# Kernel tuning notes

Hardware: AMD Instinct MI355X
Metric: run time of the kernel (lower is better)

Reference implementation:

```python
import jax, jax.numpy as jnp
import numpy as np

# dims
N, T, DIN = 256, 32, 2048      # batch, time, gpt output dim
H = 2048                        # MLP hidden
G, C, D = 2, 16, 256            # vq groups, codebook size, code dim
W, A = 5, 7                     # action window, action dim
WA = W * A                      # output_size
DEC_H = 512                     # vqvae decoder hidden
NT = N * T


def _mk(key, shape, scale=0.02):
    return jax.random.normal(key, shape, dtype=jnp.float32) * scale


def setup_inputs() -> dict:
    key = jax.random.key(0)
    ks = jax.random.split(key, 16)
    inp = {
        "x": jax.random.normal(ks[0], (N, T, DIN), dtype=jnp.float32),
        # bin1 MLP: DIN -> H -> H -> C
        "w11": _mk(ks[1], (DIN, H)), "b11": jnp.zeros((H,), jnp.float32),
        "w12": _mk(ks[2], (H, H)),   "b12": jnp.zeros((H,), jnp.float32),
        "w13": _mk(ks[3], (H, C)),   "b13": jnp.zeros((C,), jnp.float32),
        # bin2 MLP: DIN+C -> H -> C
        "w21": _mk(ks[4], (DIN + C, H)), "b21": jnp.zeros((H,), jnp.float32),
        "w22": _mk(ks[5], (H, C)),       "b22": jnp.zeros((C,), jnp.float32),
        # offset MLP: DIN -> H -> H -> G*C*WA
        "wo1": _mk(ks[6], (DIN, H)), "bo1": jnp.zeros((H,), jnp.float32),
        "wo2": _mk(ks[7], (H, H)),   "bo2": jnp.zeros((H,), jnp.float32),
        "wo3": _mk(ks[8], (H, G * C * WA)), "bo3": jnp.zeros((G * C * WA,), jnp.float32),
        # residual-VQ codebooks: (G, C, D)
        "codebook": _mk(ks[9], (G, C, D), scale=1.0),
        # frozen vqvae decoder: G*D -> DEC_H -> WA
        "wd1": _mk(ks[10], (G * D, DEC_H)), "bd1": jnp.zeros((DEC_H,), jnp.float32),
        "wd2": _mk(ks[11], (DEC_H, WA)),    "bd2": jnp.zeros((WA,), jnp.float32),
    }
    return inp


def reference(x, w11, b11, w12, b12, w13, b13, w21, b21, w22, b22,
              wo1, bo1, wo2, bo2, wo3, bo3, codebook, wd1, bd1, wd2, bd2):
    xf = x.reshape(NT, DIN)
    # bin1 logits
    h = jax.nn.relu(xf @ w11 + b11)
    h = jax.nn.relu(h @ w12 + b12)
    cbet_logits1 = h @ w13 + b13                       # (NT, C)
    # offsets
    o = jax.nn.relu(xf @ wo1 + bo1)
    o = jax.nn.relu(o @ wo2 + bo2)
    cbet_offsets = (o @ wo3 + bo3).reshape(NT, G, C, WA)
    # multinomial sampling (== categorical over softmax(logits))
    key = jax.random.key(42)
    k1, k2 = jax.random.split(key)
    s1 = jax.random.categorical(k1, cbet_logits1)      # (NT,)
    one_hot1 = jax.nn.one_hot(s1, C, dtype=xf.dtype)
    h2 = jax.nn.relu(jnp.concatenate([xf, one_hot1], axis=1) @ w21 + b21)
    cbet_logits2 = h2 @ w22 + b22                      # (NT, C)
    s2 = jax.random.categorical(k2, cbet_logits2)
    sampled_centers = jnp.stack([s1, s2], axis=1)      # (NT, G)
    # gather offsets at sampled codes, sum over groups
    nt_idx = jnp.arange(NT)[:, None]
    g_idx = jnp.arange(G)[None, :]
    sampled_offsets = cbet_offsets[nt_idx, g_idx, sampled_centers].sum(axis=1)  # (NT, WA)
    # vq codebook lookup + frozen decoder (detached in torch)
    centers = codebook[g_idx, sampled_centers]          # (NT, G, D)
    dec_in = jax.lax.stop_gradient(centers.reshape(NT, G * D))
    decoded = jax.nn.relu(dec_in @ wd1 + bd1) @ wd2 + bd2
    decoded = jax.lax.stop_gradient(decoded)            # (NT, WA)
    predicted = (decoded.reshape(NT, W, A) + sampled_offsets.reshape(NT, W, A))
    predicted_action = predicted.reshape(N, T, WA)
    return predicted_action, decoded, cbet_logits1, cbet_logits2, sampled_centers
```

## Files before the change

kernel.cpp:

```cpp
#include <hip/hip_runtime.h>
#include <cstdint>
#include <cstddef>

#define NT_   8192
#define DIN_  2048
#define H_    2048
#define C_    16
#define G_    2
#define D_    256
#define WA_   35
#define DECH_ 512
#define NPAD_ 1152

typedef _Float16 f16;
typedef _Float16 h4 __attribute__((ext_vector_type(4)));
typedef _Float16 h8 __attribute__((ext_vector_type(8)));
typedef float fx4 __attribute__((ext_vector_type(4)));

typedef __attribute__((address_space(1))) const void gvoid_t;
typedef __attribute__((address_space(3))) void lvoid_t;

__device__ __forceinline__ void gld16(const void* g, void* l) {
  __builtin_amdgcn_global_load_lds((gvoid_t*)(uintptr_t)g,
                                   (lvoid_t*)(uint32_t)(uintptr_t)l, 16, 0, 0);
}

template <int N>
__device__ __forceinline__ void waitvm() {
  if constexpr (N == 8)      asm volatile("s_waitcnt vmcnt(8)" ::: "memory");
  else if constexpr (N == 6) asm volatile("s_waitcnt vmcnt(6)" ::: "memory");
  else if constexpr (N == 4) asm volatile("s_waitcnt vmcnt(4)" ::: "memory");
  else if constexpr (N == 2) asm volatile("s_waitcnt vmcnt(2)" ::: "memory");
  else                       asm volatile("s_waitcnt vmcnt(0)" ::: "memory");
}

__host__ __device__ inline void tf2x32(uint32_t k0, uint32_t k1,
                                       uint32_t x0, uint32_t x1,
                                       uint32_t& o0, uint32_t& o1) {
  const uint32_t ks2 = k0 ^ k1 ^ 0x1BD11BDAu;
  uint32_t ks[3] = {k0, k1, ks2};
  x0 += ks[0]; x1 += ks[1];
  const uint32_t R0[4] = {13u, 15u, 26u, 6u};
  const uint32_t R1[4] = {17u, 29u, 16u, 24u};
#pragma unroll
  for (int g = 0; g < 5; ++g) {
    const uint32_t* R = (g & 1) ? R1 : R0;
#pragma unroll
    for (int r = 0; r < 4; ++r) {
      x0 += x1;
      x1 = (x1 << R[r]) | (x1 >> (32u - R[r]));
      x1 ^= x0;
    }
    x0 += ks[(g + 1) % 3];
    x1 += ks[(g + 2) % 3] + (uint32_t)(g + 1);
  }
  o0 = x0; o1 = x1;
}

template <int TERMS, int RELU, int GATHER, int WLO, int ACONV>
__global__ __launch_bounds__(512, 2) void gemm256(
    const void* __restrict__ Ahi_, const void* __restrict__ Alo_,
    const f16* __restrict__ Bhi, const f16* __restrict__ Blo,
    const float* __restrict__ bias,
    f16* __restrict__ Chi, f16* __restrict__ Clo,
    int M, int N, int K,
    const int* __restrict__ gidx, const float* __restrict__ growp, int gldw) {
  extern __shared__ f16 lds[];
  constexpr int NREG = (TERMS == 3) ? 4 : 2;
  constexpr int BS   = NREG * 8192;
  constexpr int NGLD = (TERMS == 3) ? (ACONV ? 4 : 8) : (ACONV ? 2 : 4);

  const int tid  = threadIdx.x;
  const int wave = tid >> 6;
  const int lane = tid & 63;
  const int lr   = lane & 15;

  const int nb  = N >> 8;
  const int nwg = (int)gridDim.x;
  const int qq  = nwg >> 3;
  const int sw  = ((int)blockIdx.x & 7) * qq + ((int)blockIdx.x >> 3);
  const int by  = sw / nb, bx = sw % nb;
  const int m0  = by << 8, n0 = bx << 8;

  const int wm = (wave >> 2) * 128;
  const int wn = (wave & 3) * 64;

  fx4 acc[8][4];
#pragma unroll
  for (int i = 0; i < 8; ++i)
#pragma unroll
    for (int j = 0; j < 4; ++j) acc[i][j] = (fx4){0.f, 0.f, 0.f, 0.f};

  const int r_row = wave * 16 + (lane >> 2);
  const int r_g   = (lane & 3) ^ ((lane >> 3) & 3);
  const f16* gsrc[NGLD];
  int gdst[NGLD];
  {
    int nr = 0;
    auto AR = [&](const f16* P, int mn, int reg, int rb) {
      gsrc[nr] = P + (size_t)(mn + rb + r_row) * K + r_g * 8;
      gdst[nr] = reg * 8192 + rb * 32 + wave * 512;
      ++nr;
    };
    if constexpr (TERMS == 3) {
      if constexpr (!ACONV) {
        AR((const f16*)Ahi_, m0, 0, 0); AR((const f16*)Ahi_, m0, 0, 128);
        AR((const f16*)Alo_, m0, 1, 0); AR((const f16*)Alo_, m0, 1, 128);
      }
      AR(Bhi, n0, 2, 0); AR(Bhi, n0, 2, 128);
      AR(Blo, n0, 3, 0); AR(Blo, n0, 3, 128);
    } else {
      if constexpr (!ACONV) {
        AR((const f16*)Ahi_, m0, 0, 0); AR((const f16*)Ahi_, m0, 0, 128);
      }
      AR(Bhi, n0, 1, 0); AR(Bhi, n0, 1, 128);
    }
  }

  const float* A32 = (const float*)Ahi_;
  const float* psrc[4];
  int pdst[4];
  if constexpr (ACONV) {
#pragma unroll
    for (int p = 0; p < 4; ++p) {
      const int e4 = tid + p * 512;
      const int arow = e4 >> 3;
      psrc[p] = A32 + (size_t)(m0 + arow) * K + (e4 & 7) * 4;
      const int phys = ((e4 >> 1) & 3) ^ ((e4 >> 4) & 3);
      pdst[p] = arow * 32 + phys * 8 + (e4 & 1) * 4;
    }
  }

  float4 pf[4];
  if constexpr (ACONV) {
#pragma unroll
    for (int p = 0; p < 4; ++p) pf[p] = *(const float4*)psrc[p];
  }
#pragma unroll
  for (int r = 0; r < NGLD; ++r) gld16(gsrc[r], lds + gdst[r]);

  const int KT  = K >> 5;
  const int pg8 = ((lane >> 4) ^ ((lr >> 1) & 3)) * 8;

  for (int t = 0; t < KT; ++t) {
    f16* const sb  = lds + (t & 1) * BS;
    f16* const nsb = lds + ((t + 1) & 1) * BS;
    const int ktn = (t + 1 < KT ? t + 1 : t) * 32;

    if constexpr (ACONV) {
#pragma unroll
      for (int p = 0; p < 4; ++p) {
        const float4 v = pf[p];
        h4 hh; hh.x = (f16)v.x; hh.y = (f16)v.y; hh.z = (f16)v.z; hh.w = (f16)v.w;
        *(h4*)(sb + pdst[p]) = hh;
        if constexpr (TERMS == 3) {
          h4 ll;
          ll.x = (f16)(v.x - (float)hh.x); ll.y = (f16)(v.y - (float)hh.y);
          ll.z = (f16)(v.z - (float)hh.z); ll.w = (f16)(v.w - (float)hh.w);
          *(h4*)(sb + 8192 + pdst[p]) = ll;
        }
      }
      asm volatile("s_waitcnt lgkmcnt(0)" ::: "memory");
    }
    if constexpr (ACONV) {
#pragma unroll
      for (int p = 0; p < 4; ++p) pf[p] = *(const float4*)(psrc[p] + ktn);
    }
#pragma unroll
    for (int r = 0; r < NGLD; ++r) gld16(gsrc[r] + ktn, nsb + gdst[r]);
    if constexpr (!ACONV) waitvm<NGLD>();
    __builtin_amdgcn_s_barrier();
    asm volatile("" ::: "memory");

    const f16* sAh = sb;
    const f16* sAl = sb + 8192;
    const f16* sBh = sb + (TERMS == 3 ? 2 : 1) * 8192;
    const f16* sBl = sb + 3 * 8192;

    h8 vbh[4], vbl[4];
#pragma unroll
    for (int j = 0; j < 4; ++j) {
      const int row = wn + j * 16 + lr;
      vbh[j] = *(const h8*)(sBh + row * 32 + pg8);
      if constexpr (TERMS == 3) vbl[j] = *(const h8*)(sBl + row * 32 + pg8);
    }
#pragma unroll
    for (int mq = 0; mq < 2; ++mq) {
      h8 va[4];
#pragma unroll
      for (int i = 0; i < 4; ++i)
        va[i] = *(const h8*)(sAh + (wm + mq * 64 + i * 16 + lr) * 32 + pg8);
      __builtin_amdgcn_s_setprio(1);
#pragma unroll
      for (int i = 0; i < 4; ++i)
#pragma unroll
        for (int j = 0; j < 4; ++j) {
          acc[mq * 4 + i][j] = __builtin_amdgcn_mfma_f32_16x16x32_f16(
              va[i], vbh[j], acc[mq * 4 + i][j], 0, 0, 0);
          if constexpr (TERMS == 3)
            acc[mq * 4 + i][j] = __builtin_amdgcn_mfma_f32_16x16x32_f16(
                va[i], vbl[j], acc[mq * 4 + i][j], 0, 0, 0);
        }
      __builtin_amdgcn_s_setprio(0);
      if constexpr (TERMS == 3) {
        h8 vl[4];
#pragma unroll
        for (int i = 0; i < 4; ++i)
          vl[i] = *(const h8*)(sAl + (wm + mq * 64 + i * 16 + lr) * 32 + pg8);
        __builtin_amdgcn_s_setprio(1);
#pragma unroll
        for (int i = 0; i < 4; ++i)
#pragma unroll
          for (int j = 0; j < 4; ++j)
            acc[mq * 4 + i][j] = __builtin_amdgcn_mfma_f32_16x16x32_f16(
                vl[i], vbh[j], acc[mq * 4 + i][j], 0, 0, 0);
        __builtin_amdgcn_s_setprio(0);
      }
    }
    __builtin_amdgcn_s_barrier();
    asm volatile("" ::: "memory");
  }

  const int rq = (lane >> 4) * 4;
#pragma unroll
  for (int mi = 0; mi < 8; ++mi) {
#pragma unroll
    for (int q = 0; q < 4; ++q) {
      const int row = m0 + wm + mi * 16 + rq + q;
      const float* gr = nullptr;
      if constexpr (GATHER) gr = growp + (size_t)gidx[row] * gldw;
#pragma unroll
      for (int j = 0; j < 4; ++j) {
        const int col = n0 + wn + j * 16 + lr;
        float v = acc[mi][j][q];
        if (bias) v += bias[col];
        if constexpr (GATHER) v += gr[col];
        if constexpr (RELU) v = fmaxf(v, 0.f);
        const f16 hh = (f16)v;
        Chi[(size_t)row * N + col] = hh;
        if constexpr (WLO) Clo[(size_t)row * N + col] = (f16)(v - (float)hh);
      }
    }
  }
}

template <int TERMS, int RELU, int GATHER, int WLO, int ACONV>
__global__ __launch_bounds__(256, 2) void gemm128(
    const void* __restrict__ Ahi_, const void* __restrict__ Alo_,
    const f16* __restrict__ Bhi, const f16* __restrict__ Blo,
    const float* __restrict__ bias,
    f16* __restrict__ Chi, f16* __restrict__ Clo,
    int M, int N, int K,
    const int* __restrict__ gidx, const float* __restrict__ growp, int gldw) {
  constexpr int NTILE = (TERMS == 3) ? 4 : 2;
  __shared__ f16 lds[NTILE * 4096];
  f16* sAh = lds;
  f16* sBh = lds + 4096;

  const int tid  = threadIdx.x;
  const int wave = tid >> 6;
  const int lane = tid & 63;
  const int n0 = blockIdx.x * 128;
  const int m0 = blockIdx.y * 128;
  const int wm = (wave >> 1) * 64;
  const int wn = (wave & 1) * 64;
  const int lr = lane & 15;
  const int lk = (lane >> 4) * 8;

  fx4 acc[4][4];
#pragma unroll
  for (int i = 0; i < 4; ++i)
#pragma unroll
    for (int j = 0; j < 4; ++j) acc[i][j] = (fx4){0.f, 0.f, 0.f, 0.f};

  const int sb = wave * 2048 + (lane << 4);

  for (int kt = 0; kt < K; kt += 32) {
#pragma unroll
    for (int c = 0; c < 2; ++c) {
      const int boff = sb + c * 1024;
      const int row  = boff >> 6;
      const int col  = (boff & 63) >> 1;
      gld16(Bhi + (size_t)(n0 + row) * K + kt + col, sBh + (wave * 2 + c) * 512);
      gld16(((const f16*)Ahi_) + (size_t)(m0 + row) * K + kt + col,
            sAh + (wave * 2 + c) * 512);
    }
    __syncthreads();

    h8 ah[4], bh[4];
#pragma unroll
    for (int t = 0; t < 4; ++t) {
      ah[t] = *(const h8*)&sAh[(wm + t * 16 + lr) * 32 + lk];
      bh[t] = *(const h8*)&sBh[(wn + t * 16 + lr) * 32 + lk];
    }
#pragma unroll
    for (int i = 0; i < 4; ++i)
#pragma unroll
      for (int j = 0; j < 4; ++j)
        acc[i][j] = __builtin_amdgcn_mfma_f32_16x16x32_f16(ah[i], bh[j], acc[i][j], 0, 0, 0);
    __syncthreads();
  }

  const int rq = (lane >> 4) * 4;
#pragma unroll
  for (int i = 0; i < 4; ++i) {
#pragma unroll
    for (int q = 0; q < 4; ++q) {
      const int row = m0 + wm + i * 16 + rq + q;
#pragma unroll
      for (int j = 0; j < 4; ++j) {
        const int col = n0 + wn + j * 16 + lr;
        float v = acc[i][j][q];
        if (bias) v += bias[col];
        if constexpr (RELU) v = fmaxf(v, 0.f);
        Chi[(size_t)row * N + col] = (f16)v;
      }
    }
  }
}

template <int SPLIT>
__global__ __launch_bounds__(256) void wtransT(
    const float* __restrict__ src, f16* __restrict__ hi, f16* __restrict__ lo,
    int K, int N, int Npad) {
  __shared__ float t[32][33];
  const int bn = blockIdx.x * 32;
  const int bk = blockIdx.y * 32;
  const int tx = threadIdx.x & 31, ty = threadIdx.x >> 5;
#pragma unroll
  for (int r = ty; r < 32; r += 8) {
    const float v = (bn + tx < N) ? src[(size_t)(bk + r) * N + bn + tx] : 0.f;
    t[tx][r] = v;
  }
  __syncthreads();
#pragma unroll
  for (int r = ty; r < 32; r += 8) {
    const float v = t[r][tx];
    const f16 hh = (f16)v;
    hi[(size_t)(bn + r) * K + bk + tx] = hh;
    if (SPLIT) lo[(size_t)(bn + r) * K + bk + tx] = (f16)(v - (float)hh);
  }
}

__global__ __launch_bounds__(256) void skinny16_hl(
    const f16* __restrict__ Ahi, const f16* __restrict__ Alo,
    const float* __restrict__ W, const float* __restrict__ bias,
    float* __restrict__ out) {
  __shared__ float row[H_];
  __shared__ float red[256];
  const int m = blockIdx.x;
  const f16* ah = Ahi + (size_t)m * H_;
  const f16* al = Alo + (size_t)m * H_;
  for (int i = threadIdx.x; i < H_ / 4; i += 256) {
    const h4 hh = ((const h4*)ah)[i];
    const h4 ll = ((const h4*)al)[i];
    row[i * 4 + 0] = (float)hh.x + (float)ll.x;
    row[i * 4 + 1] = (float)hh.y + (float)ll.y;
    row[i * 4 + 2] = (float)hh.z + (float)ll.z;
    row[i * 4 + 3] = (float)hh.w + (float)ll.w;
  }
  __syncthreads();
  const int c = threadIdx.x & 15, seg = threadIdx.x >> 4;
  const int k0 = seg * (H_ / 16);
  float p = 0.f;
  for (int i = 0; i < H_ / 16; ++i)
    p = fmaf(row[k0 + i], W[(size_t)(k0 + i) * C_ + c], p);
  red[threadIdx.x] = p;
  __syncthreads();
  if (threadIdx.x < C_) {
    float s = bias[threadIdx.x];
    for (int sg = 0; sg < 16; ++sg) s += red[sg * 16 + threadIdx.x];
    out[(size_t)m * C_ + threadIdx.x] = s;
  }
}

__global__ void sample_kernel(const float* __restrict__ logits,
                              int* __restrict__ s_out,
                              float* __restrict__ centers_out,
                              uint32_t ka, uint32_t kb, int which) {
  const int m = blockIdx.x * blockDim.x + threadIdx.x;
  if (m >= NT_) return;
  float best = -3.4e38f;
  int bi = 0;
#pragma unroll
  for (int c = 0; c < C_; ++c) {
    const uint32_t j = (uint32_t)(m * C_ + c);
    uint32_t o0, o1;
    tf2x32(ka, kb, 0u, j, o0, o1);
    const uint32_t bits = o0 ^ o1;
    const uint32_t fb = (bits >> 9) | 0x3f800000u;
    float u = __uint_as_float(fb) - 1.0f;
    u = fmaxf(1.17549435e-38f, u);
    const float gmb = -logf(-logf(u));
    const float z = gmb + logits[(size_t)m * C_ + c];
    if (z > best) { best = z; bi = c; }
  }
  s_out[m] = bi;
  centers_out[(size_t)m * G_ + which] = (float)bi;
}

__global__ void gather_dec_kernel(const float* __restrict__ codebook,
                                  const int* __restrict__ s1,
                                  const int* __restrict__ s2,
                                  f16* __restrict__ dec_in) {
  const int idx = blockIdx.x * blockDim.x + threadIdx.x;
  const int m = idx >> 9, d = idx & 511;
  const int g = d >> 8, dd = d & 255;
  const int s = g ? s2[m] : s1[m];
  dec_in[idx] = (f16)codebook[(size_t)(g * C_ + s) * D_ + dd];
}

__global__ __launch_bounds__(320) void final2(
    const f16* __restrict__ P,
    const float* __restrict__ bo3,
    const f16* __restrict__ dech,
    const float* __restrict__ wd2, const float* __restrict__ bd2,
    const int* __restrict__ s1, const int* __restrict__ s2,
    float* __restrict__ out_pred, float* __restrict__ out_dec) {
  __shared__ float drow[DECH_];
  const int m = blockIdx.x;
  for (int i = threadIdx.x; i < DECH_; i += 320)
    drow[i] = (float)dech[(size_t)m * DECH_ + i];
  __syncthreads();
  const int a1 = s1[m], a2 = s2[m];
  const int c = threadIdx.x >> 3, g = threadIdx.x & 7;
  float pdec = 0.f;
  if (c < WA_) {
    for (int i = 0; i < DECH_ / 8; ++i) {
      const int k = g * (DECH_ / 8) + i;
      pdec = fmaf(drow[k], wd2[(size_t)k * WA_ + c], pdec);
    }
  }
#pragma unroll
  for (int off = 1; off < 8; off <<= 1) pdec += __shfl_xor(pdec, off);
  if (c < WA_ && g == 0) {
    const float dec = pdec + bd2[c];
    const float soff = (float)P[(size_t)m * NPAD_ + a1 * WA_ + c]
                     + (float)P[(size_t)m * NPAD_ + C_ * WA_ + a2 * WA_ + c]
                     + bo3[a1 * WA_ + c] + bo3[C_ * WA_ + a2 * WA_ + c];
    out_dec[(size_t)m * WA_ + c] = dec;
    out_pred[(size_t)m * WA_ + c] = dec + soff;
  }
}

extern "C" void kernel_launch(void* const* d_in, const int* in_sizes, int n_in,
                              void* d_out, int out_size, void* d_ws, size_t ws_size,
                              hipStream_t stream) {
  const float* x    = (const float*)d_in[0];
  const float* w11  = (const float*)d_in[1];
  const float* b11  = (const float*)d_in[2];
  const float* w12  = (const float*)d_in[3];
  const float* b12  = (const float*)d_in[4];
  const float* w13  = (const float*)d_in[5];
  const float* b13  = (const float*)d_in[6];
  const float* w21  = (const float*)d_in[7];
  const float* b21  = (const float*)d_in[8];
  const float* w22  = (const float*)d_in[9];
  const float* b22  = (const float*)d_in[10];
  const float* wo1  = (const float*)d_in[11];
  const float* bo1  = (const float*)d_in[12];
  const float* wo2  = (const float*)d_in[13];
  const float* bo2  = (const float*)d_in[14];
  const float* wo3  = (const float*)d_in[15];
  const float* bo3  = (const float*)d_in[16];
  const float* cbk  = (const float*)d_in[17];
  const float* wd1  = (const float*)d_in[18];
  const float* bd1  = (const float*)d_in[19];
  const float* wd2  = (const float*)d_in[20];
  const float* bd2  = (const float*)d_in[21];

  float* out = (float*)d_out;
  float* out_pred = out;
  float* out_dec  = out + (size_t)NT_ * WA_;
  float* out_l1   = out + (size_t)2 * NT_ * WA_;
  float* out_l2   = out_l1 + (size_t)NT_ * C_;
  float* out_sc   = out_l2 + (size_t)NT_ * C_;

  const size_t AB = (size_t)NT_ * H_;
  f16* R0a = (f16*)d_ws;
  f16* R0b = R0a + AB;
  f16* R1a = R0b + AB;
  f16* R1b = R1a + AB;
  f16* WH  = R1b + AB;
  f16* WL  = WH + (size_t)H_ * H_;
  int* S1  = (int*)(WL + (size_t)H_ * H_);
  int* S2  = S1 + NT_;

  f16* P     = R1a;
  f16* DECIN = R0a;
  f16* DECH  = R0a + (size_t)NT_ * DECH_;

  hipFuncSetAttribute(reinterpret_cast<const void*>(&gemm256<3,1,0,1,1>),
                      hipFuncAttributeMaxDynamicSharedMemorySize, 131072);
  hipFuncSetAttribute(reinterpret_cast<const void*>(&gemm256<3,1,0,1,0>),
                      hipFuncAttributeMaxDynamicSharedMemorySize, 131072);
  hipFuncSetAttribute(reinterpret_cast<const void*>(&gemm256<3,1,1,1,1>),
                      hipFuncAttributeMaxDynamicSharedMemorySize, 131072);
  hipFuncSetAttribute(reinterpret_cast<const void*>(&gemm256<1,1,0,0,1>),
                      hipFuncAttributeMaxDynamicSharedMemorySize, 65536);
  hipFuncSetAttribute(reinterpret_cast<const void*>(&gemm256<1,1,0,0,0>),
                      hipFuncAttributeMaxDynamicSharedMemorySize, 65536);

  uint32_t k1a, k1b, k2a, k2b;
  tf2x32(0u, 42u, 0u, 0u, k1a, k1b);
  tf2x32(0u, 42u, 0u, 1u, k2a, k2b);

  const dim3 b256(256), b512(512);
  const dim3 gW(H_ / 32, H_ / 32);
  const dim3 gWo3(NPAD_ / 32, H_ / 32);
  const dim3 gWd1(DECH_ / 32, DECH_ / 32);
  const dim3 gBig((NT_ / 256) * (H_ / 256));
  const dim3 gP(NPAD_ / 128, NT_ / 128);
  const dim3 gD(DECH_ / 128, NT_ / 128);

  wtransT<1><<<gW, b256, 0, stream>>>(w11, WH, WL, H_, H_, H_);
  gemm256<3,1,0,1,1><<<gBig, b512, 131072, stream>>>(
      x, nullptr, WH, WL, b11, R0a, R0b, NT_, H_, DIN_, nullptr, nullptr, 0);
  wtransT<1><<<gW, b256, 0, stream>>>(w12, WH, WL, H_, H_, H_);
  gemm256<3,1,0,1,0><<<gBig, b512, 131072, stream>>>(
      R0a, R0b, WH, WL, b12, R1a, R1b, NT_, H_, H_, nullptr, nullptr, 0);
  skinny16_hl<<<NT_, 256, 0, stream>>>(R1a, R1b, w13, b13, out_l1);
  sample_kernel<<<NT_ / 256, 256, 0, stream>>>(out_l1, S1, out_sc, k1a, k1b, 0);

  wtransT<1><<<gW, b256, 0, stream>>>(w21, WH, WL, H_, H_, H_);
  gemm256<3,1,1,1,1><<<gBig, b512, 131072, stream>>>(
      x, nullptr, WH, WL, b21, R1a, R1b, NT_, H_, DIN_,
      S1, w21 + (size_t)DIN_ * H_, H_);
  skinny16_hl<<<NT_, 256, 0, stream>>>(R1a, R1b, w22, b22, out_l2);
  sample_kernel<<<NT_ / 256, 256, 0, stream>>>(out_l2, S2, out_sc, k2a, k2b, 1);

  wtransT<0><<<gW, b256, 0, stream>>>(wo1, WH, nullptr, H_, H_, H_);
  gemm256<1,1,0,0,1><<<gBig, b512, 65536, stream>>>(
      x, nullptr, WH, nullptr, bo1, R0a, nullptr, NT_, H_, DIN_, nullptr, nullptr, 0);
  wtransT<0><<<gW, b256, 0, stream>>>(wo2, WH, nullptr, H_, H_, H_);
  gemm256<1,1,0,0,0><<<gBig, b512, 65536, stream>>>(
      R0a, nullptr, WH, nullptr, bo2, R0b, nullptr, NT_, H_, H_, nullptr, nullptr, 0);
  wtransT<0><<<gWo3, b256, 0, stream>>>(wo3, WH, nullptr, H_, G_ * C_ * WA_, NPAD_);
  gemm128<1,0,0,0,0><<<gP, b256, 0, stream>>>(
      R0b, nullptr, WH, nullptr, nullptr, P, nullptr, NT_, NPAD_, H_, nullptr, nullptr, 0);

  gather_dec_kernel<<<(NT_ * DECH_) / 256, 256, 0, stream>>>(cbk, S1, S2, DECIN);
  wtransT<0><<<gWd1, b256, 0, stream>>>(wd1, WH, nullptr, DECH_, DECH_, DECH_);
  gemm128<1,1,0,0,0><<<gD, b256, 0, stream>>>(
      DECIN, nullptr, WH, nullptr, bd1, DECH, nullptr, NT_, DECH_, DECH_, nullptr, nullptr, 0);

  final2<<<NT_, 320, 0, stream>>>(P, bo3, DECH, wd2, bd2, S1, S2, out_pred, out_dec);

  (void)in_sizes; (void)n_in; (void)out_size; (void)ws_size;
}
```

Baseline: 1.102 ms.

## Pre-split x to fp16 pairs, fuse logit projection into GEMM epilogue, re-pipeline K loop

```diff
diff --git a/kernel.cpp b/kernel.cpp
--- a/kernel.cpp
+++ b/kernel.cpp
@@ -25,14 +25,13 @@
                                    (lvoid_t*)(uint32_t)(uintptr_t)l, 16, 0, 0);
 }
 
-template <int N>
-__device__ __forceinline__ void waitvm() {
-  if constexpr (N == 8)      asm volatile("s_waitcnt vmcnt(8)" ::: "memory");
-  else if constexpr (N == 6) asm volatile("s_waitcnt vmcnt(6)" ::: "memory");
-  else if constexpr (N == 4) asm volatile("s_waitcnt vmcnt(4)" ::: "memory");
-  else if constexpr (N == 2) asm volatile("s_waitcnt vmcnt(2)" ::: "memory");
-  else                       asm volatile("s_waitcnt vmcnt(0)" ::: "memory");
-}
+__device__ __forceinline__ void barrier_() {
+  asm volatile("" ::: "memory");
+  __builtin_amdgcn_s_barrier();
+  asm volatile("" ::: "memory");
+}
+
+#define MFMA_(d, a, b) d = __builtin_amdgcn_mfma_f32_16x16x32_f16(a, b, d, 0, 0, 0)
 
 __host__ __device__ inline void tf2x32(uint32_t k0, uint32_t k1,
                                        uint32_t x0, uint32_t x1,
@@ -57,18 +56,37 @@
   o0 = x0; o1 = x1;
 }
 
-template <int TERMS, int RELU, int GATHER, int WLO, int ACONV>
+__global__ __launch_bounds__(256) void xsplit_kernel(
+    const float* __restrict__ x, f16* __restrict__ xh, f16* __restrict__ xl) {
+  const size_t i = (size_t)blockIdx.x * 256 + threadIdx.x;
+  const float4 v0 = *(const float4*)(x + i * 8);
+  const float4 v1 = *(const float4*)(x + i * 8 + 4);
+  float vv[8] = {v0.x, v0.y, v0.z, v0.w, v1.x, v1.y, v1.z, v1.w};
+  h8 hh, ll;
+#pragma unroll
+  for (int k = 0; k < 8; ++k) {
+    const f16 h = (f16)vv[k];
+    hh[k] = h;
+    ll[k] = (f16)(vv[k] - (float)h);
+  }
+  *(h8*)(xh + i * 8) = hh;
+  *(h8*)(xl + i * 8) = ll;
+}
+
+enum { EPI_PAIR = 0, EPI_HI = 1, EPI_LOGIT = 2 };
+
+template <int TERMS, int GATHER, int EPI>
 __global__ __launch_bounds__(512, 2) void gemm256(
-    const void* __restrict__ Ahi_, const void* __restrict__ Alo_,
-    const f16* __restrict__ Bhi, const f16* __restrict__ Blo,
+    const f16* __restrict__ Ah, const f16* __restrict__ Al,
+    const f16* __restrict__ Bh, const f16* __restrict__ Bl,
     const float* __restrict__ bias,
     f16* __restrict__ Chi, f16* __restrict__ Clo,
     int M, int N, int K,
-    const int* __restrict__ gidx, const float* __restrict__ growp, int gldw) {
+    const int* __restrict__ gidx, const float* __restrict__ growp, int gldw,
+    const float* __restrict__ wlog, float* __restrict__ part) {
   extern __shared__ f16 lds[];
-  constexpr int NREG = (TERMS == 3) ? 4 : 2;
-  constexpr int BS   = NREG * 8192;
-  constexpr int NGLD = (TERMS == 3) ? (ACONV ? 4 : 8) : (ACONV ? 2 : 4);
+  constexpr int BS = ((TERMS == 3) ? 4 : 2) * 8192;
+  constexpr int NGLD = (TERMS == 3) ? 8 : 4;
 
   const int tid  = threadIdx.x;
   const int wave = tid >> 6;
@@ -103,157 +121,192 @@
       ++nr;
     };
     if constexpr (TERMS == 3) {
-      if constexpr (!ACONV) {
-        AR((const f16*)Ahi_, m0, 0, 0); AR((const f16*)Ahi_, m0, 0, 128);
-        AR((const f16*)Alo_, m0, 1, 0); AR((const f16*)Alo_, m0, 1, 128);
-      }
-      AR(Bhi, n0, 2, 0); AR(Bhi, n0, 2, 128);
-      AR(Blo, n0, 3, 0); AR(Blo, n0, 3, 128);
+      AR(Ah, m0, 0, 0); AR(Ah, m0, 0, 128);
+      AR(Al, m0, 1, 0); AR(Al, m0, 1, 128);
+      AR(Bh, n0, 2, 0); AR(Bh, n0, 2, 128);
+      AR(Bl, n0, 3, 0); AR(Bl, n0, 3, 128);
     } else {
-      if constexpr (!ACONV) {
-        AR((const f16*)Ahi_, m0, 0, 0); AR((const f16*)Ahi_, m0, 0, 128);
-      }
-      AR(Bhi, n0, 1, 0); AR(Bhi, n0, 1, 128);
-    }
-  }
-
-  const float* A32 = (const float*)Ahi_;
-  const float* psrc[4];
-  int pdst[4];
-  if constexpr (ACONV) {
-#pragma unroll
-    for (int p = 0; p < 4; ++p) {
-      const int e4 = tid + p * 512;
-      const int arow = e4 >> 3;
-      psrc[p] = A32 + (size_t)(m0 + arow) * K + (e4 & 7) * 4;
-      const int phys = ((e4 >> 1) & 3) ^ ((e4 >> 4) & 3);
-      pdst[p] = arow * 32 + phys * 8 + (e4 & 1) * 4;
-    }
-  }
-
-  float4 pf[4];
-  if constexpr (ACONV) {
-#pragma unroll
-    for (int p = 0; p < 4; ++p) pf[p] = *(const float4*)psrc[p];
-  }
+      AR(Ah, m0, 0, 0); AR(Ah, m0, 0, 128);
+      AR(Bh, n0, 1, 0); AR(Bh, n0, 1, 128);
+    }
+  }
+
 #pragma unroll
   for (int r = 0; r < NGLD; ++r) gld16(gsrc[r], lds + gdst[r]);
-
+  asm volatile("s_waitcnt vmcnt(0)" ::: "memory");
+  barrier_();
+
+  const int pg8 = ((lane >> 4) ^ ((lr >> 1) & 3)) * 8;
   const int KT  = K >> 5;
-  const int pg8 = ((lane >> 4) ^ ((lr >> 1) & 3)) * 8;
 
   for (int t = 0; t < KT; ++t) {
     f16* const sb  = lds + (t & 1) * BS;
     f16* const nsb = lds + ((t + 1) & 1) * BS;
     const int ktn = (t + 1 < KT ? t + 1 : t) * 32;
 
-    if constexpr (ACONV) {
-#pragma unroll
-      for (int p = 0; p < 4; ++p) {
-        const float4 v = pf[p];
-        h4 hh; hh.x = (f16)v.x; hh.y = (f16)v.y; hh.z = (f16)v.z; hh.w = (f16)v.w;
-        *(h4*)(sb + pdst[p]) = hh;
-        if constexpr (TERMS == 3) {
-          h4 ll;
-          ll.x = (f16)(v.x - (float)hh.x); ll.y = (f16)(v.y - (float)hh.y);
-          ll.z = (f16)(v.z - (float)hh.z); ll.w = (f16)(v.w - (float)hh.w);
-          *(h4*)(sb + 8192 + pdst[p]) = ll;
-        }
-      }
-      asm volatile("s_waitcnt lgkmcnt(0)" ::: "memory");
-    }
-    if constexpr (ACONV) {
-#pragma unroll
-      for (int p = 0; p < 4; ++p) pf[p] = *(const float4*)(psrc[p] + ktn);
-    }
-#pragma unroll
-    for (int r = 0; r < NGLD; ++r) gld16(gsrc[r] + ktn, nsb + gdst[r]);
-    if constexpr (!ACONV) waitvm<NGLD>();
-    __builtin_amdgcn_s_barrier();
-    asm volatile("" ::: "memory");
-
     const f16* sAh = sb;
     const f16* sAl = sb + 8192;
     const f16* sBh = sb + (TERMS == 3 ? 2 : 1) * 8192;
     const f16* sBl = sb + 3 * 8192;
 
-    h8 vbh[4], vbl[4];
+    h8 vbh[4], vbl[4], va[4];
 #pragma unroll
     for (int j = 0; j < 4; ++j) {
-      const int row = wn + j * 16 + lr;
-      vbh[j] = *(const h8*)(sBh + row * 32 + pg8);
-      if constexpr (TERMS == 3) vbl[j] = *(const h8*)(sBl + row * 32 + pg8);
-    }
-#pragma unroll
-    for (int mq = 0; mq < 2; ++mq) {
-      h8 va[4];
+      vbh[j] = *(const h8*)(sBh + (wn + j * 16 + lr) * 32 + pg8);
+      if constexpr (TERMS == 3)
+        vbl[j] = *(const h8*)(sBl + (wn + j * 16 + lr) * 32 + pg8);
+    }
+#pragma unroll
+    for (int i = 0; i < 4; ++i)
+      va[i] = *(const h8*)(sAh + (wm + i * 16 + lr) * 32 + pg8);
+    gld16(gsrc[0] + ktn, nsb + gdst[0]);
+    gld16(gsrc[1] + ktn, nsb + gdst[1]);
+    if constexpr (TERMS == 3) gld16(gsrc[2] + ktn, nsb + gdst[2]);
+    barrier_();
+    asm volatile("s_waitcnt lgkmcnt(0)" ::: "memory");
+    __builtin_amdgcn_sched_barrier(0);
+    __builtin_amdgcn_s_setprio(1);
+#pragma unroll
+    for (int i = 0; i < 4; ++i)
+#pragma unroll
+      for (int j = 0; j < 4; ++j) MFMA_(acc[i][j], va[i], vbh[j]);
+    if constexpr (TERMS == 3) {
 #pragma unroll
       for (int i = 0; i < 4; ++i)
-        va[i] = *(const h8*)(sAh + (wm + mq * 64 + i * 16 + lr) * 32 + pg8);
+#pragma unroll
+        for (int j = 0; j < 4; ++j) MFMA_(acc[i][j], va[i], vbl[j]);
+    }
+    __builtin_amdgcn_s_setprio(0);
+    barrier_();
+#pragma unroll
+    for (int i = 0; i < 4; ++i)
+      va[i] = *(const h8*)(sAh + (wm + 64 + i * 16 + lr) * 32 + pg8);
+    if constexpr (TERMS == 3) {
+      gld16(gsrc[3] + ktn, nsb + gdst[3]);
+      gld16(gsrc[4] + ktn, nsb + gdst[4]);
+      gld16(gsrc[5] + ktn, nsb + gdst[5]);
+    } else {
+      gld16(gsrc[2] + ktn, nsb + gdst[2]);
+      gld16(gsrc[3] + ktn, nsb + gdst[3]);
+    }
+    barrier_();
+    asm volatile("s_waitcnt lgkmcnt(0)" ::: "memory");
+    __builtin_amdgcn_sched_barrier(0);
+    __builtin_amdgcn_s_setprio(1);
+#pragma unroll
+    for (int i = 0; i < 4; ++i)
+#pragma unroll
+      for (int j = 0; j < 4; ++j) MFMA_(acc[4 + i][j], va[i], vbh[j]);
+    if constexpr (TERMS == 3) {
+#pragma unroll
+      for (int i = 0; i < 4; ++i)
+#pragma unroll
+        for (int j = 0; j < 4; ++j) MFMA_(acc[4 + i][j], va[i], vbl[j]);
+    }
+    __builtin_amdgcn_s_setprio(0);
+    if constexpr (TERMS != 3) asm volatile("s_waitcnt vmcnt(0)" ::: "memory");
+    barrier_();
+    if constexpr (TERMS == 3) {
+      h8 vl0[4], vl1[4];
+#pragma unroll
+      for (int i = 0; i < 4; ++i) {
+        vl0[i] = *(const h8*)(sAl + (wm + i * 16 + lr) * 32 + pg8);
+        vl1[i] = *(const h8*)(sAl + (wm + 64 + i * 16 + lr) * 32 + pg8);
+      }
+      gld16(gsrc[6] + ktn, nsb + gdst[6]);
+      gld16(gsrc[7] + ktn, nsb + gdst[7]);
+      barrier_();
+      asm volatile("s_waitcnt lgkmcnt(0)" ::: "memory");
+      __builtin_amdgcn_sched_barrier(0);
       __builtin_amdgcn_s_setprio(1);
 #pragma unroll
       for (int i = 0; i < 4; ++i)
 #pragma unroll
         for (int j = 0; j < 4; ++j) {
-          acc[mq * 4 + i][j] = __builtin_amdgcn_mfma_f32_16x16x32_f16(
-              va[i], vbh[j], acc[mq * 4 + i][j], 0, 0, 0);
-          if constexpr (TERMS == 3)
-            acc[mq * 4 + i][j] = __builtin_amdgcn_mfma_f32_16x16x32_f16(
-                va[i], vbl[j], acc[mq * 4 + i][j], 0, 0, 0);
+          MFMA_(acc[i][j], vl0[i], vbh[j]);
+          MFMA_(acc[4 + i][j], vl1[i], vbh[j]);
         }
       __builtin_amdgcn_s_setprio(0);
-      if constexpr (TERMS == 3) {
-        h8 vl[4];
-#pragma unroll
-        for (int i = 0; i < 4; ++i)
-          vl[i] = *(const h8*)(sAl + (wm + mq * 64 + i * 16 + lr) * 32 + pg8);
-        __builtin_amdgcn_s_setprio(1);
-#pragma unroll
-        for (int i = 0; i < 4; ++i)
-#pragma unroll
-          for (int j = 0; j < 4; ++j)
-            acc[mq * 4 + i][j] = __builtin_amdgcn_mfma_f32_16x16x32_f16(
-                vl[i], vbh[j], acc[mq * 4 + i][j], 0, 0, 0);
-        __builtin_amdgcn_s_setprio(0);
+      asm volatile("s_waitcnt vmcnt(0)" ::: "memory");
+      barrier_();
+    }
+  }
+
+  const int rq = (lane >> 4) * 4;
+  if constexpr (EPI == EPI_LOGIT) {
+#pragma unroll
+    for (int mi = 0; mi < 8; ++mi) {
+#pragma unroll
+      for (int q = 0; q < 4; ++q) {
+        const int row = m0 + wm + mi * 16 + rq + q;
+        const float* gr = nullptr;
+        if constexpr (GATHER) gr = growp + (size_t)gidx[row] * gldw;
+#pragma unroll
+        for (int j = 0; j < 4; ++j) {
+          const int col = n0 + wn + j * 16 + lr;
+          float v = acc[mi][j][q] + bias[col];
+          if constexpr (GATHER) v += gr[col];
+          acc[mi][j][q] = fmaxf(v, 0.f);
+        }
       }
     }
-    __builtin_amdgcn_s_barrier();
-    asm volatile("" ::: "memory");
-  }
-
-  const int rq = (lane >> 4) * 4;
-#pragma unroll
-  for (int mi = 0; mi < 8; ++mi) {
-#pragma unroll
-    for (int q = 0; q < 4; ++q) {
-      const int row = m0 + wm + mi * 16 + rq + q;
-      const float* gr = nullptr;
-      if constexpr (GATHER) gr = growp + (size_t)gidx[row] * gldw;
-#pragma unroll
-      for (int j = 0; j < 4; ++j) {
-        const int col = n0 + wn + j * 16 + lr;
-        float v = acc[mi][j][q];
-        if (bias) v += bias[col];
-        if constexpr (GATHER) v += gr[col];
-        if constexpr (RELU) v = fmaxf(v, 0.f);
-        const f16 hh = (f16)v;
-        Chi[(size_t)row * N + col] = hh;
-        if constexpr (WLO) Clo[(size_t)row * N + col] = (f16)(v - (float)hh);
+    const int sidx = bx * 4 + (wave & 3);
+    float* pout = part + ((size_t)sidx * NT_ + (m0 + wm)) * 16;
+    const int qw = lr >> 2, cw = lr & 3;
+#pragma unroll
+    for (int cc = 0; cc < 4; ++cc) {
+      float4 wv[4];
+#pragma unroll
+      for (int j = 0; j < 4; ++j)
+        wv[j] = *(const float4*)(wlog + (size_t)(n0 + wn + j * 16 + lr) * 16 + cc * 4);
+#pragma unroll
+      for (int mi = 0; mi < 8; ++mi) {
+        float pl[4][4] = {{0.f}};
+#pragma unroll
+        for (int j = 0; j < 4; ++j)
+#pragma unroll
+          for (int q = 0; q < 4; ++q) {
+            pl[q][0] += acc[mi][j][q] * wv[j].x;
+            pl[q][1] += acc[mi][j][q] * wv[j].y;
+            pl[q][2] += acc[mi][j][q] * wv[j].z;
+            pl[q][3] += acc[mi][j][q] * wv[j].w;
+          }
+#pragma unroll
+        for (int st = 1; st < 16; st <<= 1) {
+#pragma unroll
+          for (int q = 0; q < 4; ++q)
+#pragma unroll
+            for (int c = 0; c < 4; ++c) pl[q][c] += __shfl_xor(pl[q][c], st);
+        }
+        pout[(size_t)(mi * 16 + rq + qw) * 16 + cc * 4 + cw] = pl[qw][cw];
       }
     }
-  }
-}
-
-template <int TERMS, int RELU, int GATHER, int WLO, int ACONV>
+  } else {
+#pragma unroll
+    for (int mi = 0; mi < 8; ++mi) {
+#pragma unroll
+      for (int q = 0; q < 4; ++q) {
+        const int row = m0 + wm + mi * 16 + rq + q;
+#pragma unroll
+        for (int j = 0; j < 4; ++j) {
+          const int col = n0 + wn + j * 16 + lr;
+          float v = fmaxf(acc[mi][j][q] + bias[col], 0.f);
+          const f16 hh = (f16)v;
+          Chi[(size_t)row * N + col] = hh;
+          if constexpr (EPI == EPI_PAIR)
+            Clo[(size_t)row * N + col] = (f16)(v - (float)hh);
+        }
+      }
+    }
+  }
+}
+
+template <int RELU>
 __global__ __launch_bounds__(256, 2) void gemm128(
-    const void* __restrict__ Ahi_, const void* __restrict__ Alo_,
-    const f16* __restrict__ Bhi, const f16* __restrict__ Blo,
-    const float* __restrict__ bias,
-    f16* __restrict__ Chi, f16* __restrict__ Clo,
-    int M, int N, int K,
-    const int* __restrict__ gidx, const float* __restrict__ growp, int gldw) {
-  constexpr int NTILE = (TERMS == 3) ? 4 : 2;
-  __shared__ f16 lds[NTILE * 4096];
+    const f16* __restrict__ Ah, const f16* __restrict__ Bh,
+    const float* __restrict__ bias, f16* __restrict__ Chi,
+    int M, int N, int K) {
+  __shared__ f16 lds[2 * 4096];
   f16* sAh = lds;
   f16* sBh = lds + 4096;
 
@@ -281,9 +334,8 @@
       const int boff = sb + c * 1024;
       const int row  = boff >> 6;
       const int col  = (boff & 63) >> 1;
-      gld16(Bhi + (size_t)(n0 + row) * K + kt + col, sBh + (wave * 2 + c) * 512);
-      gld16(((const f16*)Ahi_) + (size_t)(m0 + row) * K + kt + col,
-            sAh + (wave * 2 + c) * 512);
+      gld16(Bh + (size_t)(n0 + row) * K + kt + col, sBh + (wave * 2 + c) * 512);
+      gld16(Ah + (size_t)(m0 + row) * K + kt + col, sAh + (wave * 2 + c) * 512);
     }
     __syncthreads();
 
@@ -296,8 +348,7 @@
 #pragma unroll
     for (int i = 0; i < 4; ++i)
 #pragma unroll
-      for (int j = 0; j < 4; ++j)
-        acc[i][j] = __builtin_amdgcn_mfma_f32_16x16x32_f16(ah[i], bh[j], acc[i][j], 0, 0, 0);
+      for (int j = 0; j < 4; ++j) MFMA_(acc[i][j], ah[i], bh[j]);
     __syncthreads();
   }
 
@@ -342,61 +393,35 @@
   }
 }
 
-__global__ __launch_bounds__(256) void skinny16_hl(
-    const f16* __restrict__ Ahi, const f16* __restrict__ Alo,
-    const float* __restrict__ W, const float* __restrict__ bias,
-    float* __restrict__ out) {
-  __shared__ float row[H_];
-  __shared__ float red[256];
-  const int m = blockIdx.x;
-  const f16* ah = Ahi + (size_t)m * H_;
-  const f16* al = Alo + (size_t)m * H_;
-  for (int i = threadIdx.x; i < H_ / 4; i += 256) {
-    const h4 hh = ((const h4*)ah)[i];
-    const h4 ll = ((const h4*)al)[i];
-    row[i * 4 + 0] = (float)hh.x + (float)ll.x;
-    row[i * 4 + 1] = (float)hh.y + (float)ll.y;
-    row[i * 4 + 2] = (float)hh.z + (float)ll.z;
-    row[i * 4 + 3] = (float)hh.w + (float)ll.w;
-  }
-  __syncthreads();
-  const int c = threadIdx.x & 15, seg = threadIdx.x >> 4;
-  const int k0 = seg * (H_ / 16);
-  float p = 0.f;
-  for (int i = 0; i < H_ / 16; ++i)
-    p = fmaf(row[k0 + i], W[(size_t)(k0 + i) * C_ + c], p);
-  red[threadIdx.x] = p;
-  __syncthreads();
-  if (threadIdx.x < C_) {
-    float s = bias[threadIdx.x];
-    for (int sg = 0; sg < 16; ++sg) s += red[sg * 16 + threadIdx.x];
-    out[(size_t)m * C_ + threadIdx.x] = s;
-  }
-}
-
-__global__ void sample_kernel(const float* __restrict__ logits,
-                              int* __restrict__ s_out,
-                              float* __restrict__ centers_out,
-                              uint32_t ka, uint32_t kb, int which) {
-  const int m = blockIdx.x * blockDim.x + threadIdx.x;
-  if (m >= NT_) return;
-  float best = -3.4e38f;
-  int bi = 0;
-#pragma unroll
-  for (int c = 0; c < C_; ++c) {
-    const uint32_t j = (uint32_t)(m * C_ + c);
-    uint32_t o0, o1;
-    tf2x32(ka, kb, 0u, j, o0, o1);
-    const uint32_t bits = o0 ^ o1;
-    const uint32_t fb = (bits >> 9) | 0x3f800000u;
-    float u = __uint_as_float(fb) - 1.0f;
-    u = fmaxf(1.17549435e-38f, u);
-    const float gmb = -logf(-logf(u));
-    const float z = gmb + logits[(size_t)m * C_ + c];
-    if (z > best) { best = z; bi = c; }
-  }
-  s_out[m] = bi;
-  centers_out[(size_t)m * G_ + which] = (float)bi;
+__global__ __launch_bounds__(256) void reduce_sample(
+    const float* __restrict__ part, const float* __restrict__ bias,
+    float* __restrict__ logits_out, int* __restrict__ s_out,
+    float* __restrict__ centers_out, uint32_t ka, uint32_t kb, int which) {
+  const int tid = threadIdx.x;
+  const int c = tid & 15;
+  const int m = blockIdx.x * 16 + (tid >> 4);
+  float v = bias[c];
+#pragma unroll 8
+  for (int s = 0; s < 32; ++s) v += part[((size_t)s * NT_ + m) * 16 + c];
+  logits_out[(size_t)m * C_ + c] = v;
+  const uint32_t j = (uint32_t)(m * C_ + c);
+  uint32_t o0, o1;
+  tf2x32(ka, kb, 0u, j, o0, o1);
+  const uint32_t bits = o0 ^ o1;
+  float u = __uint_as_float((bits >> 9) | 0x3f800000u) - 1.0f;
+  u = fmaxf(1.17549435e-38f, u);
+  float z = -logf(-logf(u)) + v;
+  int bi = c;
+#pragma unroll
+  for (int st = 1; st < 16; st <<= 1) {
+    const float oz = __shfl_xor(z, st);
+    const int   ob = __shfl_xor(bi, st);
+    if (oz > z || (oz == z && ob < bi)) { z = oz; bi = ob; }
+  }
+  if (c == 0) {
+    s_out[m] = bi;
+    centers_out[(size_t)m * G_ + which] = (float)bi;
+  }
 }
 
 __global__ void gather_dec_kernel(const float* __restrict__ codebook,
@@ -477,28 +502,29 @@
   float* out_sc   = out_l2 + (size_t)NT_ * C_;
 
   const size_t AB = (size_t)NT_ * H_;
-  f16* R0a = (f16*)d_ws;
-  f16* R0b = R0a + AB;
-  f16* R1a = R0b + AB;
-  f16* R1b = R1a + AB;
-  f16* WH  = R1b + AB;
-  f16* WL  = WH + (size_t)H_ * H_;
-  int* S1  = (int*)(WL + (size_t)H_ * H_);
-  int* S2  = S1 + NT_;
-
-  f16* P     = R1a;
-  f16* DECIN = R0a;
-  f16* DECH  = R0a + (size_t)NT_ * DECH_;
-
-  hipFuncSetAttribute(reinterpret_cast<const void*>(&gemm256<3,1,0,1,1>),
+  f16*   Xh   = (f16*)d_ws;
+  f16*   Xl   = Xh + AB;
+  f16*   H1a  = Xl + AB;
+  f16*   H1b  = H1a + AB;
+  f16*   WH   = H1b + AB;
+  f16*   WL   = WH + (size_t)H_ * H_;
+  float* PART = (float*)(WL + (size_t)H_ * H_);
+  int*   S1   = (int*)(PART + (size_t)32 * NT_ * C_);
+  int*   S2   = S1 + NT_;
+
+  f16* O1    = H1a;
+  f16* O2    = H1b;
+  f16* P     = Xh;
+  f16* DECIN = Xl;
+  f16* DECH  = Xl + (size_t)NT_ * DECH_;
+
+  hipFuncSetAttribute(reinterpret_cast<const void*>(&gemm256<3,0,EPI_PAIR>),
                       hipFuncAttributeMaxDynamicSharedMemorySize, 131072);
-  hipFuncSetAttribute(reinterpret_cast<const void*>(&gemm256<3,1,0,1,0>),
+  hipFuncSetAttribute(reinterpret_cast<const void*>(&gemm256<3,0,EPI_LOGIT>),
                       hipFuncAttributeMaxDynamicSharedMemorySize, 131072);
-  hipFuncSetAttribute(reinterpret_cast<const void*>(&gemm256<3,1,1,1,1>),
+  hipFuncSetAttribute(reinterpret_cast<const void*>(&gemm256<3,1,EPI_LOGIT>),
                       hipFuncAttributeMaxDynamicSharedMemorySize, 131072);
-  hipFuncSetAttribute(reinterpret_cast<const void*>(&gemm256<1,1,0,0,1>),
-                      hipFuncAttributeMaxDynamicSharedMemorySize, 65536);
-  hipFuncSetAttribute(reinterpret_cast<const void*>(&gemm256<1,1,0,0,0>),
+  hipFuncSetAttribute(reinterpret_cast<const void*>(&gemm256<1,0,EPI_HI>),
                       hipFuncAttributeMaxDynamicSharedMemorySize, 65536);
 
   uint32_t k1a, k1b, k2a, k2b;
@@ -513,38 +539,43 @@
   const dim3 gP(NPAD_ / 128, NT_ / 128);
   const dim3 gD(DECH_ / 128, NT_ / 128);
 
+  xsplit_kernel<<<NT_ * H_ / (8 * 256), b256, 0, stream>>>(x, Xh, Xl);
+
   wtransT<1><<<gW, b256, 0, stream>>>(w11, WH, WL, H_, H_, H_);
-  gemm256<3,1,0,1,1><<<gBig, b512, 131072, stream>>>(
-      x, nullptr, WH, WL, b11, R0a, R0b, NT_, H_, DIN_, nullptr, nullptr, 0);
+  gemm256<3,0,EPI_PAIR><<<gBig, b512, 131072, stream>>>(
+      Xh, Xl, WH, WL, b11, H1a, H1b, NT_, H_, DIN_,
+      nullptr, nullptr, 0, nullptr, nullptr);
   wtransT<1><<<gW, b256, 0, stream>>>(w12, WH, WL, H_, H_, H_);
-  gemm256<3,1,0,1,0><<<gBig, b512, 131072, stream>>>(
-      R0a, R0b, WH, WL, b12, R1a, R1b, NT_, H_, H_, nullptr, nullptr, 0);
-  skinny16_hl<<<NT_, 256, 0, stream>>>(R1a, R1b, w13, b13, out_l1);
-  sample_kernel<<<NT_ / 256, 256, 0, stream>>>(out_l1, S1, out_sc, k1a, k1b, 0);
+  gemm256<3,0,EPI_LOGIT><<<gBig, b512, 131072, stream>>>(
+      H1a, H1b, WH, WL, b12, nullptr, nullptr, NT_, H_, H_,
+      nullptr, nullptr, 0, w13, PART);
+  reduce_sample<<<NT_ / 16, b256, 0, stream>>>(PART, b13, out_l1, S1, out_sc,
+                                               k1a, k1b, 0);
 
   wtransT<1><<<gW, b256, 0, stream>>>(w21, WH, WL, H_, H_, H_);
-  gemm256<3,1,1,1,1><<<gBig, b512, 131072, stream>>>(
-      x, nullptr, WH, WL, b21, R1a, R1b, NT_, H_, DIN_,
-      S1, w21 + (size_t)DIN_ * H_, H_);
-  skinny16_hl<<<NT_, 256, 0, stream>>>(R1a, R1b, w22, b22, out_l2);
-  sample_kernel<<<NT_ / 256, 256, 0, stream>>>(out_l2, S2, out_sc, k2a, k2b, 1);
+  gemm256<3,1,EPI_LOGIT><<<gBig, b512, 131072, stream>>>(
+      Xh, Xl, WH, WL, b21, nullptr, nullptr, NT_, H_, DIN_,
+      S1, w21 + (size_t)DIN_ * H_, H_, w22, PART);
+  reduce_sample<<<NT_ / 16, b256, 0, stream>>>(PART, b22, out_l2, S2, out_sc,
+                                               k2a, k2b, 1);
 
   wtransT<0><<<gW, b256, 0, stream>>>(wo1, WH, nullptr, H_, H_, H_);
-  gemm256<1,1,0,0,1><<<gBig, b512, 65536, stream>>>(
-      x, nullptr, WH, nullptr, bo1, R0a, nullptr, NT_, H_, DIN_, nullptr, nullptr, 0);
+  gemm256<1,0,EPI_HI><<<gBig, b512, 65536, stream>>>(
+      Xh, nullptr, WH, nullptr, bo1, O1, nullptr, NT_, H_, DIN_,
+      nullptr, nullptr, 0, nullptr, nullptr);
   wtransT<0><<<gW, b256, 0, stream>>>(wo2, WH, nullptr, H_, H_, H_);
-  gemm256<1,1,0,0,0><<<gBig, b512, 65536, stream>>>(
-      R0a, nullptr, WH, nullptr, bo2, R0b, nullptr, NT_, H_, H_, nullptr, nullptr, 0);
+  gemm256<1,0,EPI_HI><<<gBig, b512, 65536, stream>>>(
+      O1, nullptr, WH, nullptr, bo2, O2, nullptr, NT_, H_, H_,
+      nullptr, nullptr, 0, nullptr, nullptr);
   wtransT<0><<<gWo3, b256, 0, stream>>>(wo3, WH, nullptr, H_, G_ * C_ * WA_, NPAD_);
-  gemm128<1,0,0,0,0><<<gP, b256, 0, stream>>>(
-      R0b, nullptr, WH, nullptr, nullptr, P, nullptr, NT_, NPAD_, H_, nullptr, nullptr, 0);
-
-  gather_dec_kernel<<<(NT_ * DECH_) / 256, 256, 0, stream>>>(cbk, S1, S2, DECIN);
+  gemm128<0><<<gP, b256, 0, stream>>>(O2, WH, nullptr, P, NT_, NPAD_, H_);
+
+  gather_dec_kernel<<<(NT_ * DECH_) / 256, b256, 0, stream>>>(cbk, S1, S2, DECIN);
   wtransT<0><<<gWd1, b256, 0, stream>>>(wd1, WH, nullptr, DECH_, DECH_, DECH_);
-  gemm128<1,1,0,0,0><<<gD, b256, 0, stream>>>(
-      DECIN, nullptr, WH, nullptr, bd1, DECH, nullptr, NT_, DECH_, DECH_, nullptr, nullptr, 0);
-
-  final2<<<NT_, 320, 0, stream>>>(P, bo3, DECH, wd2, bd2, S1, S2, out_pred, out_dec);
+  gemm128<1><<<gD, b256, 0, stream>>>(DECIN, WH, bd1, DECH, NT_, DECH_, DECH_);
+
+  final2<<<NT_, 320, 0, stream>>>(P, bo3, DECH, wd2, bd2, S1, S2,
+                                  out_pred, out_dec);
 
   (void)in_sizes; (void)n_in; (void)out_size; (void)ws_size;
 }
```

New measurement: 1.064 ms. 1.04x faster.
